# Kernel tuning notes

Measured on AMD Instinct MI355X. Metric: run time of the kernel, lower is better.

Reference implementation:

```python
import jax, jax.numpy as jnp
import numpy as np

B, N1, N2 = 16, 512, 512
F1 = F2 = 1024
HID = 512
DEG = 32           # candidate matches per (batch,row) -> nnz = B*N1*DEG
NNZ = B * N1 * DEG


def setup_inputs() -> dict:
    key = jax.random.key(0)
    ks = jax.random.split(key, 8)
    t1 = jax.random.normal(ks[0], (B, N1, F1), jnp.float32)
    t2 = jax.random.normal(ks[1], (B, N2, F2), jnp.float32)
    # Sparse indicator H: every (b, i) row has exactly DEG nonzeros so each
    # softmax segment is nonempty (matches a real matching indicator matrix).
    idx_b = jnp.repeat(jnp.arange(B, dtype=jnp.int32), N1 * DEG)
    idx_i = jnp.tile(jnp.repeat(jnp.arange(N1, dtype=jnp.int32), DEG), B)
    idx_j = jax.random.randint(ks[2], (NNZ,), 0, N2, dtype=jnp.int32)
    # Learned params (nn.Linear stores weight as (out, in))
    s1 = 1.0 / np.sqrt(F1)
    s2 = 1.0 / np.sqrt(F2)
    W1 = jax.random.uniform(ks[3], (HID, F1), jnp.float32, -s1, s1)
    b1 = jax.random.uniform(ks[4], (HID,), jnp.float32, -s1, s1)
    W2 = jax.random.uniform(ks[5], (HID, F2), jnp.float32, -s2, s2)
    b2 = jax.random.uniform(ks[6], (HID,), jnp.float32, -s2, s2)
    v = jax.random.uniform(ks[7], (HID,), jnp.float32, -1.0 / HID, 1.0 / HID)
    return {"t1": t1, "t2": t2, "idx_b": idx_b, "idx_i": idx_i, "idx_j": idx_j,
            "W1": W1, "b1": b1, "W2": W2, "b2": b2, "v": v}


def reference(t1, t2, idx_b, idx_i, idx_j, W1, b1, W2, b2, v):
    # Dense projections (GEMMs)
    q1 = jnp.einsum('bnf,hf->bnh', t1, W1) + b1   # (B, N1, HID)
    q2 = jnp.einsum('bnf,hf->bnh', t2, W2) + b2   # (B, N2, HID)
    # Gather to sparse pattern: x._values() = q1[b,i] + q2[b,j]
    vals = q1[idx_b, idx_i] + q2[idx_b, idx_j]    # (NNZ, HID)
    w = vals @ v                                  # (NNZ,)
    # Segment softmax per (batch, row) group — replaces the nested loops
    seg = idx_b.astype(jnp.int32) * N1 + idx_i.astype(jnp.int32)
    nseg = B * N1
    m = jax.ops.segment_max(w, seg, num_segments=nseg)
    e = jnp.exp(w - m[seg])
    s = jax.ops.segment_sum(e, seg, num_segments=nseg)
    return e / s[seg]                             # sparse values of w_softmax
```

## Files before the change

### kernel.cpp

```cpp
#include <hip/hip_runtime.h>

#define B_    16
#define N1_   512
#define N2_   512
#define F_    1024
#define HID_  512
#define DEG_  32
#define NNZ_  (B_ * N1_ * DEG_)
#define NROWS (B_ * N2_)


__global__ __launch_bounds__(256) void k_partial(
        const float* __restrict__ W2,
        const float* __restrict__ v,
        float* __restrict__ partial) {
    const int cb = blockIdx.x & 3;
    const int rb = blockIdx.x >> 2;
    const int f  = cb * 256 + threadIdx.x;

    __shared__ float vs[64];
    if (threadIdx.x < 64) vs[threadIdx.x] = v[rb * 64 + threadIdx.x];
    __syncthreads();

    const float* w = W2 + (size_t)rb * 64 * F_ + f;
    float acc = 0.f;
    #pragma unroll 8
    for (int h = 0; h < 64; ++h) acc += w[(size_t)h * F_] * vs[h];
    partial[rb * F_ + f] = acc;
}

__global__ __launch_bounds__(256) void k_rowdot(
        const float* __restrict__ t2,
        const float* __restrict__ partial,
        float* __restrict__ s2) {
    __shared__ float u[F_];

    const float4* p4 = (const float4*)partial;
    float4 a4 = make_float4(0.f, 0.f, 0.f, 0.f);
    #pragma unroll
    for (int rb = 0; rb < 8; ++rb) {
        float4 t = p4[rb * 256 + threadIdx.x];
        a4.x += t.x; a4.y += t.y; a4.z += t.z; a4.w += t.w;
    }
    ((float4*)u)[threadIdx.x] = a4;
    __syncthreads();

    const int wave = threadIdx.x >> 6;
    const int lane = threadIdx.x & 63;

    #pragma unroll
    for (int rr = 0; rr < 2; ++rr) {
        const int r = blockIdx.x * 8 + wave * 2 + rr;
        const float4* row = (const float4*)(t2 + (size_t)r * F_);
        float acc = 0.f;
        #pragma unroll
        for (int k = 0; k < 4; ++k) {
            const int c = k * 64 + lane;
            float4 raw = row[c];
            const float* uf = &u[c * 4];
            acc += raw.x * uf[0];
            acc += raw.y * uf[1];
            acc += raw.z * uf[2];
            acc += raw.w * uf[3];
        }
        #pragma unroll
        for (int off = 32; off >= 1; off >>= 1) acc += __shfl_xor(acc, off, 64);
        if (lane == 0) s2[r] = acc;
    }
}

__global__ __launch_bounds__(256) void k_softmax(
        const int* __restrict__ idx_b,
        const int* __restrict__ idx_j,
        const float* __restrict__ s2,
        float* __restrict__ out) {
    const int n = blockIdx.x * 256 + threadIdx.x;
    const int b = idx_b[n];
    const int j = idx_j[n];
    const float w = s2[b * N2_ + j];

    float m = w;
    #pragma unroll
    for (int off = 16; off >= 1; off >>= 1) m = fmaxf(m, __shfl_xor(m, off, 32));
    const float e = __expf(w - m);
    float s = e;
    #pragma unroll
    for (int off = 16; off >= 1; off >>= 1) s += __shfl_xor(s, off, 32);
    out[n] = e / s;
}

extern "C" void kernel_launch(void* const* d_in, const int* in_sizes, int n_in,
                              void* d_out, int out_size, void* d_ws, size_t ws_size,
                              hipStream_t stream) {
    const float* t2    = (const float*)d_in[1];
    const int*   idx_b = (const int*)d_in[2];
    const int*   idx_j = (const int*)d_in[4];
    const float* W2    = (const float*)d_in[7];
    const float* v     = (const float*)d_in[9];

    float* partial = (float*)d_ws;
    float* s2      = partial + 8 * F_;

    k_partial<<<32,          256, 0, stream>>>(W2, v, partial);
    k_rowdot <<<NROWS / 8,   256, 0, stream>>>(t2, partial, s2);
    k_softmax<<<NNZ_ / 256,  256, 0, stream>>>(idx_b, idx_j, s2,
                                               (float*)d_out);
}
```

Baseline: 112.3 us.

## Fuse projection, row-dot and softmax into one cooperative kernel with grid syncs

Merges the three kernels into a single cooperative launch of 1024 blocks that separates the phases with grid-wide barriers. The W2ᵀv reduction is reorganised so each block computes one feature column across all hidden units, which removes the separate partial-sum buffer. The goal is to eliminate inter-kernel launch gaps. In exchange it adds grid.sync overhead, relies on every block being co-resident, and uses column-strided W2 reads. A fallback to three kernels runs if the cooperative launch fails.

Result: slower. 324.5 us (+189.0%).

```diff
diff --git a/kernel.cpp b/kernel.cpp
--- a/kernel.cpp
+++ b/kernel.cpp
@@ -1,4 +1,7 @@
 #include <hip/hip_runtime.h>
+#include <hip/hip_cooperative_groups.h>
+
+namespace cg = cooperative_groups;
 
 #define B_    16
 #define N1_   512
@@ -8,46 +11,108 @@
 #define DEG_  32
 #define NNZ_  (B_ * N1_ * DEG_)
 #define NROWS (B_ * N2_)
+#define GRID_ 1024
 
 
-__global__ __launch_bounds__(256) void k_partial(
+__global__ __launch_bounds__(256, 4) void k_fused(
         const float* __restrict__ W2,
         const float* __restrict__ v,
-        float* __restrict__ partial) {
-    const int cb = blockIdx.x & 3;
-    const int rb = blockIdx.x >> 2;
-    const int f  = cb * 256 + threadIdx.x;
+        const float* __restrict__ t2,
+        const int*   __restrict__ idx_b,
+        const int*   __restrict__ idx_j,
+        float* __restrict__ u2,
+        float* __restrict__ s2,
+        float* __restrict__ out) {
+    cg::grid_group grid = cg::this_grid();
+    const int tid  = threadIdx.x;
+    const int wave = tid >> 6;
+    const int lane = tid & 63;
 
-    __shared__ float vs[64];
-    if (threadIdx.x < 64) vs[threadIdx.x] = v[rb * 64 + threadIdx.x];
-    __syncthreads();
+    __shared__ float u[F_];
+    __shared__ float red[4];
 
-    const float* w = W2 + (size_t)rb * 64 * F_ + f;
-    float acc = 0.f;
-    #pragma unroll 8
-    for (int h = 0; h < 64; ++h) acc += w[(size_t)h * F_] * vs[h];
-    partial[rb * F_ + f] = acc;
+    {
+        const int f = blockIdx.x;
+        float acc = W2[(size_t)tid * F_ + f] * v[tid]
+                  + W2[(size_t)(tid + 256) * F_ + f] * v[tid + 256];
+        #pragma unroll
+        for (int off = 32; off >= 1; off >>= 1) acc += __shfl_xor(acc, off, 64);
+        if (lane == 0) red[wave] = acc;
+        __syncthreads();
+        if (tid == 0) u2[f] = red[0] + red[1] + red[2] + red[3];
+    }
+
+    grid.sync();
+
+    {
+        ((float4*)u)[tid] = ((const float4*)u2)[tid];
+        __syncthreads();
+        #pragma unroll
+        for (int rr = 0; rr < 2; ++rr) {
+            const int r = blockIdx.x * 8 + wave * 2 + rr;
+            const float4* row = (const float4*)(t2 + (size_t)r * F_);
+            float acc = 0.f;
+            #pragma unroll
+            for (int k = 0; k < 4; ++k) {
+                const int c = k * 64 + lane;
+                float4 raw = row[c];
+                const float* uf = &u[c * 4];
+                acc += raw.x * uf[0];
+                acc += raw.y * uf[1];
+                acc += raw.z * uf[2];
+                acc += raw.w * uf[3];
+            }
+            #pragma unroll
+            for (int off = 32; off >= 1; off >>= 1) acc += __shfl_xor(acc, off, 64);
+            if (lane == 0) s2[r] = acc;
+        }
+    }
+
+    grid.sync();
+
+    {
+        const int n = blockIdx.x * 256 + tid;
+        const int b = idx_b[n];
+        const int j = idx_j[n];
+        const float w = s2[b * N2_ + j];
+        float m = w;
+        #pragma unroll
+        for (int off = 16; off >= 1; off >>= 1) m = fmaxf(m, __shfl_xor(m, off, 32));
+        const float e = __expf(w - m);
+        float s = e;
+        #pragma unroll
+        for (int off = 16; off >= 1; off >>= 1) s += __shfl_xor(s, off, 32);
+        out[n] = e / s;
+    }
 }
 
-__global__ __launch_bounds__(256) void k_rowdot(
-        const float* __restrict__ t2,
-        const float* __restrict__ partial,
+
+__global__ __launch_bounds__(256) void k_u2(
+        const float* __restrict__ W2, const float* __restrict__ v,
+        float* __restrict__ u2) {
+    const int tid  = threadIdx.x;
+    const int wave = tid >> 6;
+    const int lane = tid & 63;
+    __shared__ float red[4];
+    const int f = blockIdx.x;
+    float acc = W2[(size_t)tid * F_ + f] * v[tid]
+              + W2[(size_t)(tid + 256) * F_ + f] * v[tid + 256];
+    #pragma unroll
+    for (int off = 32; off >= 1; off >>= 1) acc += __shfl_xor(acc, off, 64);
+    if (lane == 0) red[wave] = acc;
+    __syncthreads();
+    if (tid == 0) u2[f] = red[0] + red[1] + red[2] + red[3];
+}
+
+__global__ __launch_bounds__(256) void k_rowdot2(
+        const float* __restrict__ t2, const float* __restrict__ u2,
         float* __restrict__ s2) {
     __shared__ float u[F_];
-
-    const float4* p4 = (const float4*)partial;
-    float4 a4 = make_float4(0.f, 0.f, 0.f, 0.f);
-    #pragma unroll
-    for (int rb = 0; rb < 8; ++rb) {
-        float4 t = p4[rb * 256 + threadIdx.x];
-        a4.x += t.x; a4.y += t.y; a4.z += t.z; a4.w += t.w;
-    }
-    ((float4*)u)[threadIdx.x] = a4;
+    const int tid  = threadIdx.x;
+    const int wave = tid >> 6;
+    const int lane = tid & 63;
+    ((float4*)u)[tid] = ((const float4*)u2)[tid];
     __syncthreads();
-
-    const int wave = threadIdx.x >> 6;
-    const int lane = threadIdx.x & 63;
-
     #pragma unroll
     for (int rr = 0; rr < 2; ++rr) {
         const int r = blockIdx.x * 8 + wave * 2 + rr;
@@ -70,15 +135,12 @@
 }
 
 __global__ __launch_bounds__(256) void k_softmax(
-        const int* __restrict__ idx_b,
-        const int* __restrict__ idx_j,
-        const float* __restrict__ s2,
-        float* __restrict__ out) {
+        const int* __restrict__ idx_b, const int* __restrict__ idx_j,
+        const float* __restrict__ s2, float* __restrict__ out) {
     const int n = blockIdx.x * 256 + threadIdx.x;
     const int b = idx_b[n];
     const int j = idx_j[n];
     const float w = s2[b * N2_ + j];
-
     float m = w;
     #pragma unroll
     for (int off = 16; off >= 1; off >>= 1) m = fmaxf(m, __shfl_xor(m, off, 32));
@@ -98,11 +160,18 @@
     const float* W2    = (const float*)d_in[7];
     const float* v     = (const float*)d_in[9];
 
-    float* partial = (float*)d_ws;
-    float* s2      = partial + 8 * F_;
+    float* u2  = (float*)d_ws;
+    float* s2  = u2 + F_;
+    float* out = (float*)d_out;
 
-    k_partial<<<32,          256, 0, stream>>>(W2, v, partial);
-    k_rowdot <<<NROWS / 8,   256, 0, stream>>>(t2, partial, s2);
-    k_softmax<<<NNZ_ / 256,  256, 0, stream>>>(idx_b, idx_j, s2,
-                                               (float*)d_out);
+    void* args[] = {(void*)&W2, (void*)&v, (void*)&t2, (void*)&idx_b,
+                    (void*)&idx_j, (void*)&u2, (void*)&s2, (void*)&out};
+    hipError_t err = hipLaunchCooperativeKernel(
+        (const void*)k_fused, dim3(GRID_), dim3(256), args, 0, stream);
+
+    if (err != hipSuccess) {
+        k_u2     <<<F_,         256, 0, stream>>>(W2, v, u2);
+        k_rowdot2<<<NROWS / 8,  256, 0, stream>>>(t2, u2, s2);
+        k_softmax<<<NNZ_ / 256, 256, 0, stream>>>(idx_b, idx_j, s2, out);
+    }
 }
```
